# Performance work log

Measured on AMD Instinct MI355X. Metric: run time of the kernel, lower is better.

## Reference

```python
import jax, jax.numpy as jnp
import numpy as np

# --- hash-grid / Field hyperparams (from init_kwargs defaults) ---
L = 16            # n_levels
F = 2             # n_features_per_level
LOG2_T = 19
T = 1 << LOG2_T   # hashmap size per level
NMIN = 16         # base_resolution
MAXRES = 512
SCALE = 1.0
HIDDEN = 32
OUT_DIM = 1
N = 2_000_000
B = float(np.exp(np.log(MAXRES * SCALE / NMIN) / (L - 1)))  # per_level_scale
PRIMES = jnp.array([1, 2654435761, 805459861], dtype=jnp.uint32)
# 8 corner offsets of the unit cube, (8,3)
CORNERS = jnp.array([[(c >> 0) & 1, (c >> 1) & 1, (c >> 2) & 1] for c in range(8)], dtype=jnp.uint32)


def hash_encode(xn, table):
    """xn: (N,3) in [0,1]; table: (L,T,F). Returns (N, L*F)."""
    feats = []
    for l in range(L):  # fixed small loop over levels
        s = NMIN * (B ** l) - 1.0          # tcnn-style grid scale
        pos = xn * s                        # (N,3)
        p0 = jnp.floor(pos)
        w = pos - p0                        # trilinear fracs, (N,3)
        p0i = p0.astype(jnp.uint32)
        corner = p0i[:, None, :] + CORNERS[None, :, :]          # (N,8,3)
        h = corner * PRIMES                                      # (N,8,3) uint32 wrap-mul
        idx = (h[..., 0] ^ h[..., 1] ^ h[..., 2]) & jnp.uint32(T - 1)  # (N,8)
        # trilinear weights per corner: prod over dims of w or (1-w)
        cw = jnp.where(CORNERS[None, :, :] == 1, w[:, None, :], 1.0 - w[:, None, :])
        cw = cw.prod(axis=-1)                                    # (N,8)
        g = table[l][idx.astype(jnp.int32)]                      # (N,8,F)
        feats.append(jnp.einsum('ncf,nc->nf', g, cw))            # (N,F)
    return jnp.concatenate(feats, axis=-1)                       # (N, L*F)


def setup_inputs() -> dict:
    key = jax.random.key(0)
    ks = jax.random.split(key, 8)
    x = jax.random.uniform(ks[0], (N, 3), jnp.float32)  # coords in [0,1) subset of [-scale,scale]
    table = jax.random.normal(ks[1], (L, T, F), jnp.float32) * 1e-2
    W0 = jax.random.normal(ks[2], (L * F + 3, HIDDEN), jnp.float32) * 0.1
    b0 = jnp.zeros((HIDDEN,), jnp.float32)
    W1 = jax.random.normal(ks[3], (HIDDEN, HIDDEN), jnp.float32) * 0.1
    b1 = jnp.zeros((HIDDEN,), jnp.float32)
    Wout = jax.random.normal(ks[4], (HIDDEN, OUT_DIM), jnp.float32) * 0.1
    bout = jnp.zeros((OUT_DIM,), jnp.float32)
    return {"x": x, "table": table, "W0": W0, "b0": b0, "W1": W1, "b1": b1, "Wout": Wout, "bout": bout}


def reference(x, table, W0, b0, W1, b1, Wout, bout):
    # density(): normalize coords to [0,1]
    xn = (x + SCALE) / (2.0 * SCALE)
    # back_prop=0: encoder sees detached coords
    h = hash_encode(jax.lax.stop_gradient(xn), table)   # (N, L*F)
    feat = jnp.concatenate([xn, h], axis=-1)            # (N, 35)  torch.cat([x, h], 1)
    h1 = jax.nn.elu(feat @ W0 + b0)
    h2 = jax.nn.elu(h1 @ W1 + b1)
    out = h2 @ Wout + bout                              # (N, 1)
    return out
```

## Files before the change

kernel.cpp:

```cpp
#include <hip/hip_runtime.h>
#include <hip/hip_fp16.h>
#include <cmath>

#define LVL   16
#define NDENSE 11
#define NHASH  (LVL - NDENSE)
#define TSIZE (1u << 19)
#define TMASK (TSIZE - 1u)
#define HID   32
#define PRIME1 2654435761u
#define PRIME2 805459861u
#define FSTRIDE 72

struct Scales { float s[LVL]; };
struct DenseInfo {
    int X0[NDENSE];
    int dim[NDENSE];
    int dimsq[NDENSE];
    int base[NDENSE];
    int eoff[NDENSE + 1];
};

typedef _Float16 f16x8 __attribute__((ext_vector_type(8)));
typedef float    f32x4 __attribute__((ext_vector_type(4)));
typedef float    f32x2 __attribute__((ext_vector_type(2)));
typedef unsigned u32x4 __attribute__((ext_vector_type(4)));

__device__ __forceinline__ float elu_f(float v) {
    return v > 0.0f ? v : expm1f(v);
}
__device__ __forceinline__ unsigned sel4(u32x4 v, unsigned s) {
    unsigned lo = (s & 1) ? v.y : v.x;
    unsigned hi = (s & 1) ? v.w : v.z;
    return (s & 2) ? hi : lo;
}
__device__ __forceinline__ unsigned hashed(unsigned cx, unsigned cy, unsigned cz) {
    return (cx ^ (cy * PRIME1) ^ (cz * PRIME2)) & TMASK;
}

__device__ __forceinline__ unsigned enc8(float v) {
    unsigned short t = __half_as_ushort(__float2half_rn(v * 0.0625f));
    unsigned m = (unsigned)(t & 0x7FFF) + 0x40u;
    return ((t >> 8) & 0x80u) | (m >> 7);
}
__device__ __forceinline__ float2 dec2(unsigned hw) {
    unsigned h2 = ((hw & 0x8000u) << 16) | ((hw & 0x7F00u) << 15)
                | ((hw & 0x80u)   << 8)  | ((hw & 0x7Fu)   << 7);
    __half2 hh; __builtin_memcpy(&hh, &h2, 4);
    return __half22float2(hh);
}

__global__ __launch_bounds__(256)
void convert_hash8(const f32x2* __restrict__ src, unsigned short* __restrict__ dst)
{
    int i = blockIdx.x * blockDim.x + threadIdx.x;
    if (i >= NHASH * (int)TSIZE) return;
    int l = NDENSE + i / (int)TSIZE;
    int s = i & (int)TMASK;
    f32x2 v = src[(size_t)l * TSIZE + s];
    dst[i] = (unsigned short)(enc8(v.x) | (enc8(v.y) << 8));
}

__global__ __launch_bounds__(256)
void dense_prep8(const float* __restrict__ table, u32x4* __restrict__ dtab,
                 DenseInfo di)
{
    int e = blockIdx.x * blockDim.x + threadIdx.x;
    if (e >= di.eoff[NDENSE]) return;
    int l = 0;
#pragma unroll
    for (int k = 1; k < NDENSE; ++k) if (e >= di.eoff[k]) l = k;
    int le = e - di.eoff[l];
    int D = di.dim[l];
    int ex = le % D; int r = le / D;
    int ey = r % D;  int ez = r / D;
    unsigned cx = (unsigned)(di.X0[l] + ex);
    unsigned cy = (unsigned)(di.X0[l] + ey);
    unsigned cz = (unsigned)(di.X0[l] + ez);
    const f32x2* __restrict__ tl = (const f32x2*)table + (size_t)l * TSIZE;
    f32x2 c0 = tl[hashed(cx,      cy,      cz)];
    f32x2 c1 = tl[hashed(cx + 1u, cy,      cz)];
    f32x2 c2 = tl[hashed(cx,      cy + 1u, cz)];
    f32x2 c3 = tl[hashed(cx + 1u, cy + 1u, cz)];
    f32x2 c4 = tl[hashed(cx,      cy,      cz + 1u)];
    f32x2 c5 = tl[hashed(cx + 1u, cy,      cz + 1u)];
    f32x2 c6 = tl[hashed(cx,      cy + 1u, cz + 1u)];
    f32x2 c7 = tl[hashed(cx + 1u, cy + 1u, cz + 1u)];
    u32x4 q;
    q.x = enc8(c0.x) | (enc8(c0.y) << 8) | (enc8(c1.x) << 16) | (enc8(c1.y) << 24);
    q.y = enc8(c2.x) | (enc8(c2.y) << 8) | (enc8(c3.x) << 16) | (enc8(c3.y) << 24);
    q.z = enc8(c4.x) | (enc8(c4.y) << 8) | (enc8(c5.x) << 16) | (enc8(c5.y) << 24);
    q.w = enc8(c6.x) | (enc8(c6.y) << 8) | (enc8(c7.x) << 16) | (enc8(c7.y) << 24);
    dtab[di.base[l] + le] = q;
}

__global__ void prep_frags(const float* __restrict__ W0, const float* __restrict__ W1,
                           const float* __restrict__ Wout, _Float16* __restrict__ frags)
{
    int idx = blockIdx.x * blockDim.x + threadIdx.x;
    if (idx >= 14*64*8) return;
    int f = idx >> 9;
    int rem = idx & 511;
    int lane = rem >> 3;
    int j = rem & 7;
    int q = lane >> 4;
    int nn = lane & 15;

    float w = 0.0f;
    bool lo;
    if (f < 8) {
        int part = f >> 2, kt = (f >> 1) & 1, nt = f & 1;
        int k = kt*32 + q*8 + j;
        int ncol = nt*16 + nn;
        float val = 0.0f;
        if (k < 32)      val = W0[(3 + k)  * HID + ncol];
        else if (k < 35) val = W0[(k - 32) * HID + ncol];
        else if (k < 38) val = W0[(k - 35) * HID + ncol];
        w = val; lo = (part == 1);
    } else if (f < 12) {
        int part = (f - 8) >> 1, nt = (f - 8) & 1;
        int k = q*8 + j;
        int ncol = nt*16 + nn;
        w = W1[k * HID + ncol]; lo = (part == 1);
    } else {
        int part = f - 12;
        int k = q*8 + j;
        w = (nn == 0) ? Wout[k] : 0.0f; lo = (part == 1);
    }
    _Float16 hi = (_Float16)w;
    frags[idx] = lo ? (_Float16)(w - (float)hi) : hi;
}

__global__ __launch_bounds__(256, 4)
void fused_mfma_kernel(const float* __restrict__ x, const u32x4* __restrict__ htab8,
                       const u32x4* __restrict__ dtab,
                       const float* __restrict__ b0, const float* __restrict__ b1,
                       const float* __restrict__ bout, const _Float16* __restrict__ fragbuf,
                       float* __restrict__ out, int n, Scales sc, DenseInfo di)
{
    __shared__ __attribute__((aligned(16))) _Float16 featL[256 * FSTRIDE];
    __shared__ __attribute__((aligned(16))) _Float16 h1h[4][16*32], h1l[4][16*32];
    __shared__ __attribute__((aligned(16))) _Float16 h2h[4][16*32], h2l[4][16*32];

    const int t = threadIdx.x;
    const int pbase = blockIdx.x * 256;
    const int p  = pbase + t;
    const int pc = p < n ? p : n - 1;

    const float xn0 = (x[3*pc+0] + 1.0f) * 0.5f;
    const float xn1 = (x[3*pc+1] + 1.0f) * 0.5f;
    const float xn2 = (x[3*pc+2] + 1.0f) * 0.5f;

    _Float16* row = &featL[t * FSTRIDE];
    {
        _Float16 h0 = (_Float16)xn0, h1_ = (_Float16)xn1, h2_ = (_Float16)xn2;
        row[32] = h0; row[33] = h1_; row[34] = h2_;
        row[35] = (_Float16)(xn0 - (float)h0);
        row[36] = (_Float16)(xn1 - (float)h1_);
        row[37] = (_Float16)(xn2 - (float)h2_);
#pragma unroll
        for (int k = 38; k < 64; ++k) row[k] = (_Float16)0.0f;
    }

#pragma unroll
    for (int l = 0; l < NDENSE; ++l) {
        const float s = sc.s[l];
        float px = xn0 * s, py = xn1 * s, pz = xn2 * s;
        float fx = floorf(px), fy = floorf(py), fz = floorf(pz);
        float wx = px - fx, wy = py - fy, wz = pz - fz;
        int D = di.dim[l], Dsq = di.dimsq[l], X0 = di.X0[l];
        int cx = (int)fx - X0, cy = (int)fy - X0, cz = (int)fz - X0;
        cx = min(max(cx, 0), D - 1);
        cy = min(max(cy, 0), D - 1);
        cz = min(max(cz, 0), D - 1);
        u32x4 Q = dtab[(size_t)(di.base[l] + cx + cy * D + cz * Dsq)];
        float2 a00 = dec2(Q.x & 0xFFFFu), a10 = dec2(Q.x >> 16);
        float2 a01 = dec2(Q.y & 0xFFFFu), a11 = dec2(Q.y >> 16);
        float2 c00 = dec2(Q.z & 0xFFFFu), c10 = dec2(Q.z >> 16);
        float2 c01 = dec2(Q.w & 0xFFFFu), c11 = dec2(Q.w >> 16);
        float ux = 1.0f - wx, uy = 1.0f - wy, uz = 1.0f - wz;
        float b0x = uy*(ux*a00.x + wx*a10.x) + wy*(ux*a01.x + wx*a11.x);
        float b0y = uy*(ux*a00.y + wx*a10.y) + wy*(ux*a01.y + wx*a11.y);
        float b1x = uy*(ux*c00.x + wx*c10.x) + wy*(ux*c01.x + wx*c11.x);
        float b1y = uy*(ux*c00.y + wx*c10.y) + wy*(ux*c01.y + wx*c11.y);
        row[2*l + 0] = (_Float16)(16.0f * (uz * b0x + wz * b1x));
        row[2*l + 1] = (_Float16)(16.0f * (uz * b0y + wz * b1y));
    }

#pragma unroll
    for (int l = NDENSE; l < LVL; ++l) {
        const u32x4* __restrict__ qt = htab8 + ((size_t)(l - NDENSE) * TSIZE >> 3);
        const float s = sc.s[l];
        float px = xn0 * s, py = xn1 * s, pz = xn2 * s;
        float fx = floorf(px), fy = floorf(py), fz = floorf(pz);
        float wx = px - fx, wy = py - fy, wz = pz - fz;
        unsigned x0 = (unsigned)fx, y0 = (unsigned)fy, z0 = (unsigned)fz;
        unsigned hy0 = y0 * PRIME1, hy1 = hy0 + PRIME1;
        unsigned hz0 = z0 * PRIME2, hz1 = hz0 + PRIME2;
        unsigned b00 = hy0 ^ hz0, b10 = hy1 ^ hz0, b01 = hy0 ^ hz1, b11 = hy1 ^ hz1;
        unsigned i0 = (x0 ^ b00) & TMASK;
        unsigned i1 = (x0 ^ b10) & TMASK;
        unsigned i2 = (x0 ^ b01) & TMASK;
        unsigned i3 = (x0 ^ b11) & TMASK;

        u32x4 Q0 = qt[i0 >> 3];
        u32x4 Q1 = qt[i1 >> 3];
        u32x4 Q2 = qt[i2 >> 3];
        u32x4 Q3 = qt[i3 >> 3];

        unsigned dm = (x0 ^ (x0 + 1u)) & TMASK;
        unsigned j0 = i0 ^ dm, j1 = i1 ^ dm, j2 = i2 ^ dm, j3 = i3 ^ dm;

        unsigned hc0, hc1, hc2, hc3;
        if ((x0 & 7u) == 7u) {
            u32x4 R0 = qt[j0 >> 3];
            u32x4 R1 = qt[j1 >> 3];
            u32x4 R2 = qt[j2 >> 3];
            u32x4 R3 = qt[j3 >> 3];
            unsigned d0 = sel4(R0, (j0 >> 1) & 3), d1 = sel4(R1, (j1 >> 1) & 3);
            unsigned d2 = sel4(R2, (j2 >> 1) & 3), d3 = sel4(R3, (j3 >> 1) & 3);
            hc0 = (j0 & 1) ? (d0 >> 16) : (d0 & 0xFFFFu);
            hc1 = (j1 & 1) ? (d1 >> 16) : (d1 & 0xFFFFu);
            hc2 = (j2 & 1) ? (d2 >> 16) : (d2 & 0xFFFFu);
            hc3 = (j3 & 1) ? (d3 >> 16) : (d3 & 0xFFFFu);
        } else {
            unsigned d0 = sel4(Q0, (j0 >> 1) & 3), d1 = sel4(Q1, (j1 >> 1) & 3);
            unsigned d2 = sel4(Q2, (j2 >> 1) & 3), d3 = sel4(Q3, (j3 >> 1) & 3);
            hc0 = (j0 & 1) ? (d0 >> 16) : (d0 & 0xFFFFu);
            hc1 = (j1 & 1) ? (d1 >> 16) : (d1 & 0xFFFFu);
            hc2 = (j2 & 1) ? (d2 >> 16) : (d2 & 0xFFFFu);
            hc3 = (j3 & 1) ? (d3 >> 16) : (d3 & 0xFFFFu);
        }
        unsigned e0 = sel4(Q0, (i0 >> 1) & 3), e1 = sel4(Q1, (i1 >> 1) & 3);
        unsigned e2 = sel4(Q2, (i2 >> 1) & 3), e3 = sel4(Q3, (i3 >> 1) & 3);
        unsigned ha0 = (i0 & 1) ? (e0 >> 16) : (e0 & 0xFFFFu);
        unsigned ha1 = (i1 & 1) ? (e1 >> 16) : (e1 & 0xFFFFu);
        unsigned ha2 = (i2 & 1) ? (e2 >> 16) : (e2 & 0xFFFFu);
        unsigned ha3 = (i3 & 1) ? (e3 >> 16) : (e3 & 0xFFFFu);

        float2 A0 = dec2(ha0), A1 = dec2(ha1), A2 = dec2(ha2), A3 = dec2(ha3);
        float2 C0 = dec2(hc0), C1 = dec2(hc1), C2 = dec2(hc2), C3 = dec2(hc3);
        float ux = 1.0f - wx, uy = 1.0f - wy, uz = 1.0f - wz;
        float w00 = uy*uz, w10 = wy*uz, w01 = uy*wz, w11 = wy*wz;
        float f0 = ux * (w00*A0.x + w10*A1.x + w01*A2.x + w11*A3.x)
                 + wx * (w00*C0.x + w10*C1.x + w01*C2.x + w11*C3.x);
        float f1 = ux * (w00*A0.y + w10*A1.y + w01*A2.y + w11*A3.y)
                 + wx * (w00*C0.y + w10*C1.y + w01*C2.y + w11*C3.y);

        row[2*l + 0] = (_Float16)(16.0f * f0);
        row[2*l + 1] = (_Float16)(16.0f * f1);
    }
    __syncthreads();

    const int l = t & 63, w = t >> 6;
    const int q = l >> 4, nn = l & 15;

    const f16x8* FB = (const f16x8*)fragbuf;
    f16x8 B0h00 = FB[0*64 + l], B0h01 = FB[1*64 + l];
    f16x8 B0h10 = FB[2*64 + l], B0h11 = FB[3*64 + l];
    f16x8 B0l00 = FB[4*64 + l], B0l01 = FB[5*64 + l];
    f16x8 B0l10 = FB[6*64 + l], B0l11 = FB[7*64 + l];
    f16x8 B1h0  = FB[8*64 + l], B1h1  = FB[9*64 + l];
    f16x8 B1l0  = FB[10*64 + l], B1l1 = FB[11*64 + l];
    f16x8 B2h   = FB[12*64 + l], B2l  = FB[13*64 + l];

    float bias00 = b0[nn], bias01 = b0[16 + nn];
    float bias10 = b1[nn], bias11 = b1[16 + nn];
    float biasO  = (nn == 0) ? bout[0] : 0.0f;

    _Float16* H1h = &h1h[w][0]; _Float16* H1l = &h1l[w][0];
    _Float16* H2h = &h2h[w][0]; _Float16* H2l = &h2l[w][0];

#pragma unroll
    for (int mt = 0; mt < 4; ++mt) {
        const int mrow = w*64 + mt*16 + nn;
        const _Float16* arow = &featL[mrow * FSTRIDE];

        f16x8 A0 = *(const f16x8*)(arow + q*8);
        f16x8 A1 = *(const f16x8*)(arow + 32 + q*8);
        f32x4 c0 = {bias00, bias00, bias00, bias00};
        f32x4 c1 = {bias01, bias01, bias01, bias01};
        c0 = __builtin_amdgcn_mfma_f32_16x16x32_f16(A0, B0h00, c0, 0, 0, 0);
        c0 = __builtin_amdgcn_mfma_f32_16x16x32_f16(A1, B0h10, c0, 0, 0, 0);
        c0 = __builtin_amdgcn_mfma_f32_16x16x32_f16(A0, B0l00, c0, 0, 0, 0);
        c0 = __builtin_amdgcn_mfma_f32_16x16x32_f16(A1, B0l10, c0, 0, 0, 0);
        c1 = __builtin_amdgcn_mfma_f32_16x16x32_f16(A0, B0h01, c1, 0, 0, 0);
        c1 = __builtin_amdgcn_mfma_f32_16x16x32_f16(A1, B0h11, c1, 0, 0, 0);
        c1 = __builtin_amdgcn_mfma_f32_16x16x32_f16(A0, B0l01, c1, 0, 0, 0);
        c1 = __builtin_amdgcn_mfma_f32_16x16x32_f16(A1, B0l11, c1, 0, 0, 0);

#pragma unroll
        for (int r = 0; r < 4; ++r) {
            int m = q*4 + r;
            float e0 = elu_f(c0[r]);
            _Float16 hh = (_Float16)e0;
            H1h[m*32 + nn]      = hh;
            H1l[m*32 + nn]      = (_Float16)(e0 - (float)hh);
            float e1 = elu_f(c1[r]);
            hh = (_Float16)e1;
            H1h[m*32 + 16 + nn] = hh;
            H1l[m*32 + 16 + nn] = (_Float16)(e1 - (float)hh);
        }

        f16x8 Ah = *(const f16x8*)(H1h + nn*32 + q*8);
        f16x8 Al = *(const f16x8*)(H1l + nn*32 + q*8);
        f32x4 d0 = {bias10, bias10, bias10, bias10};
        f32x4 d1 = {bias11, bias11, bias11, bias11};
        d0 = __builtin_amdgcn_mfma_f32_16x16x32_f16(Ah, B1h0, d0, 0, 0, 0);
        d0 = __builtin_amdgcn_mfma_f32_16x16x32_f16(Ah, B1l0, d0, 0, 0, 0);
        d0 = __builtin_amdgcn_mfma_f32_16x16x32_f16(Al, B1h0, d0, 0, 0, 0);
        d1 = __builtin_amdgcn_mfma_f32_16x16x32_f16(Ah, B1h1, d1, 0, 0, 0);
        d1 = __builtin_amdgcn_mfma_f32_16x16x32_f16(Ah, B1l1, d1, 0, 0, 0);
        d1 = __builtin_amdgcn_mfma_f32_16x16x32_f16(Al, B1h1, d1, 0, 0, 0);

#pragma unroll
        for (int r = 0; r < 4; ++r) {
            int m = q*4 + r;
            float e0 = elu_f(d0[r]);
            _Float16 hh = (_Float16)e0;
            H2h[m*32 + nn]      = hh;
            H2l[m*32 + nn]      = (_Float16)(e0 - (float)hh);
            float e1 = elu_f(d1[r]);
            hh = (_Float16)e1;
            H2h[m*32 + 16 + nn] = hh;
            H2l[m*32 + 16 + nn] = (_Float16)(e1 - (float)hh);
        }

        f16x8 A2h = *(const f16x8*)(H2h + nn*32 + q*8);
        f16x8 A2l = *(const f16x8*)(H2l + nn*32 + q*8);
        f32x4 c3 = {biasO, biasO, biasO, biasO};
        c3 = __builtin_amdgcn_mfma_f32_16x16x32_f16(A2h, B2h, c3, 0, 0, 0);
        c3 = __builtin_amdgcn_mfma_f32_16x16x32_f16(A2h, B2l, c3, 0, 0, 0);
        c3 = __builtin_amdgcn_mfma_f32_16x16x32_f16(A2l, B2h, c3, 0, 0, 0);

        if (nn == 0) {
            int pout = pbase + w*64 + mt*16 + q*4;
#pragma unroll
            for (int r = 0; r < 4; ++r)
                if (pout + r < n) out[pout + r] = c3[r];
        }
    }
}

__device__ __forceinline__ float2 enc_level_f32(float xn0, float xn1, float xn2, float s,
                                                const float2* __restrict__ tb)
{
    float px = xn0 * s, py = xn1 * s, pz = xn2 * s;
    float fx = floorf(px), fy = floorf(py), fz = floorf(pz);
    float wx = px - fx, wy = py - fy, wz = pz - fz;
    unsigned x0 = (unsigned)fx, y0 = (unsigned)fy, z0 = (unsigned)fz;
    unsigned hy0 = y0 * PRIME1, hy1 = hy0 + PRIME1;
    unsigned hz0 = z0 * PRIME2, hz1 = hz0 + PRIME2;
    unsigned b00 = hy0 ^ hz0, b10 = hy1 ^ hz0, b01 = hy0 ^ hz1, b11 = hy1 ^ hz1;
    float2 g000 = tb[( x0       ^ b00) & TMASK];
    float2 g100 = tb[((x0 + 1u) ^ b00) & TMASK];
    float2 g010 = tb[( x0       ^ b10) & TMASK];
    float2 g110 = tb[((x0 + 1u) ^ b10) & TMASK];
    float2 g001 = tb[( x0       ^ b01) & TMASK];
    float2 g101 = tb[((x0 + 1u) ^ b01) & TMASK];
    float2 g011 = tb[( x0       ^ b11) & TMASK];
    float2 g111 = tb[((x0 + 1u) ^ b11) & TMASK];
    float ux = 1.0f - wx, uy = 1.0f - wy, uz = 1.0f - wz;
    float c00 = uy*uz, c10 = wy*uz, c01 = uy*wz, c11 = wy*wz;
    float f0 = ux * (c00*g000.x + c10*g010.x + c01*g001.x + c11*g011.x)
             + wx * (c00*g100.x + c10*g110.x + c01*g101.x + c11*g111.x);
    float f1 = ux * (c00*g000.y + c10*g010.y + c01*g001.y + c11*g011.y)
             + wx * (c00*g100.y + c10*g110.y + c01*g101.y + c11*g111.y);
    return make_float2(f0, f1);
}

__global__ __launch_bounds__(256, 4)
void fused_fp32_kernel(const float* __restrict__ x, const float* __restrict__ table,
                       const float* __restrict__ W0, const float* __restrict__ b0,
                       const float* __restrict__ W1, const float* __restrict__ b1,
                       const float* __restrict__ Wout, const float* __restrict__ bout,
                       float* __restrict__ out, int n, Scales sc)
{
    int tid = blockIdx.x * blockDim.x + threadIdx.x;
    if (tid >= n) return;
    float xn0 = (x[3*tid+0] + 1.0f) * 0.5f;
    float xn1 = (x[3*tid+1] + 1.0f) * 0.5f;
    float xn2 = (x[3*tid+2] + 1.0f) * 0.5f;
    float acc[HID];
#pragma unroll
    for (int j = 0; j < HID; ++j)
        acc[j] = b0[j] + xn0 * W0[0*HID + j] + xn1 * W0[1*HID + j] + xn2 * W0[2*HID + j];
#pragma unroll
    for (int lv = 0; lv < LVL; ++lv) {
        const float2* tb = (const float2*)table + (size_t)lv * TSIZE;
        float2 f = enc_level_f32(xn0, xn1, xn2, sc.s[lv], tb);
        const float* w0r0 = W0 + (3 + 2*lv) * HID;
        const float* w0r1 = W0 + (4 + 2*lv) * HID;
#pragma unroll
        for (int j = 0; j < HID; ++j)
            acc[j] += f.x * w0r0[j] + f.y * w0r1[j];
    }
#pragma unroll
    for (int j = 0; j < HID; ++j) acc[j] = elu_f(acc[j]);
    float acc2[HID];
#pragma unroll
    for (int j = 0; j < HID; ++j) acc2[j] = b1[j];
#pragma unroll
    for (int k = 0; k < HID; ++k) {
        float hk = acc[k];
        const float* w1r = W1 + k * HID;
#pragma unroll
        for (int j = 0; j < HID; ++j) acc2[j] += hk * w1r[j];
    }
    float o = bout[0];
#pragma unroll
    for (int k = 0; k < HID; ++k) o += elu_f(acc2[k]) * Wout[k];
    out[tid] = o;
}

extern "C" void kernel_launch(void* const* d_in, const int* in_sizes, int n_in,
                              void* d_out, int out_size, void* d_ws, size_t ws_size,
                              hipStream_t stream)
{
    const float* x    = (const float*)d_in[0];
    const float* tb   = (const float*)d_in[1];
    const float* W0   = (const float*)d_in[2];
    const float* b0   = (const float*)d_in[3];
    const float* W1   = (const float*)d_in[4];
    const float* b1   = (const float*)d_in[5];
    const float* Wout = (const float*)d_in[6];
    const float* bo   = (const float*)d_in[7];
    float* out = (float*)d_out;

    int n = in_sizes[0] / 3;

    Scales sc;
    DenseInfo di;
    double B = exp(log(32.0) / 15.0);
    {
        int base = 0, ecum = 0;
        for (int l = 0; l < LVL; ++l) {
            double sd = 16.0 * pow(B, (double)l) - 1.0;
            sc.s[l] = (float)sd;
            if (l < NDENSE) {
                int X0   = (int)floor(0.5 * sd) - 2; if (X0 < 0) X0 = 0;
                int Xmax = (int)ceil(sd) + 2;
                int dim  = Xmax - X0 + 1;
                di.X0[l] = X0; di.dim[l] = dim; di.dimsq[l] = dim * dim;
                di.base[l] = base; di.eoff[l] = ecum;
                base += dim * dim * dim;
                ecum += dim * dim * dim;
            }
        }
        di.eoff[NDENSE] = ecum;
    }

    const size_t dense_bytes = (size_t)di.eoff[NDENSE] * 16;
    const size_t hash8_bytes = (size_t)NHASH * TSIZE * 2;
    const size_t frag_bytes  = 14 * 64 * 8 * sizeof(_Float16);
    int block = 256;
    int pgrid = (n + block - 1) / block;

    if (ws_size >= dense_bytes + hash8_bytes + frag_bytes) {
        u32x4*          dtab  = (u32x4*)d_ws;
        unsigned short* htab8 = (unsigned short*)((char*)d_ws + dense_bytes);
        _Float16*       frags = (_Float16*)((char*)d_ws + dense_bytes + hash8_bytes);
        int hgrid = (NHASH * (int)TSIZE + block - 1) / block;
        convert_hash8<<<hgrid, block, 0, stream>>>((const f32x2*)tb, htab8);
        int dgrid = (di.eoff[NDENSE] + block - 1) / block;
        dense_prep8<<<dgrid, block, 0, stream>>>(tb, dtab, di);
        prep_frags<<<28, 256, 0, stream>>>(W0, W1, Wout, frags);
        fused_mfma_kernel<<<pgrid, block, 0, stream>>>(x, (const u32x4*)htab8, dtab,
                                                       b0, b1, bo, frags, out, n, sc, di);
    } else {
        fused_fp32_kernel<<<pgrid, block, 0, stream>>>(x, tb, W0, b0, W1, b1, Wout, bo, out, n, sc);
    }
}
```

Measured before the change: 522.7 us.

## Switch tables to hardware FP8, software-pipeline hash loads, split dense table build

Table entries are now encoded with the hardware FP8 pack/unpack conversion instructions instead of the hand-rolled 8-bit half truncation. The dense-level build is split into a per-grid-point kernel followed by a cell-gather kernel, which uses the output buffer as scratch. In the main kernel, all dense-level loads are issued up front and the hash-level loads are software-pipelined three levels deep with 32-bit gathers. The feature tile uses an XOR-swizzled 64-wide layout written as 16-byte vectors, the second hidden layer reuses the first layer's LDS buffers, and ELU uses fast __expf. Together these aim to cut memory latency, preprocessing gathers, LDS bank conflicts and ALU work, at the cost of more registers and changed precision.

```diff
diff --git a/kernel.cpp b/kernel.cpp
--- a/kernel.cpp
+++ b/kernel.cpp
@@ -10,7 +10,6 @@
 #define HID   32
 #define PRIME1 2654435761u
 #define PRIME2 805459861u
-#define FSTRIDE 72
 
 struct Scales { float s[LVL]; };
 struct DenseInfo {
@@ -20,6 +19,11 @@
     int base[NDENSE];
     int eoff[NDENSE + 1];
 };
+struct PtInfo {
+    int P1[NDENSE];
+    int pbase[NDENSE];
+    int ptotal;
+};
 
 typedef _Float16 f16x8 __attribute__((ext_vector_type(8)));
 typedef float    f32x4 __attribute__((ext_vector_type(4)));
@@ -27,27 +31,28 @@
 typedef unsigned u32x4 __attribute__((ext_vector_type(4)));
 
 __device__ __forceinline__ float elu_f(float v) {
-    return v > 0.0f ? v : expm1f(v);
-}
-__device__ __forceinline__ unsigned sel4(u32x4 v, unsigned s) {
-    unsigned lo = (s & 1) ? v.y : v.x;
-    unsigned hi = (s & 1) ? v.w : v.z;
-    return (s & 2) ? hi : lo;
+    return v > 0.0f ? v : __expf(v) - 1.0f;
 }
 __device__ __forceinline__ unsigned hashed(unsigned cx, unsigned cy, unsigned cz) {
     return (cx ^ (cy * PRIME1) ^ (cz * PRIME2)) & TMASK;
 }
 
-__device__ __forceinline__ unsigned enc8(float v) {
-    unsigned short t = __half_as_ushort(__float2half_rn(v * 0.0625f));
-    unsigned m = (unsigned)(t & 0x7FFF) + 0x40u;
-    return ((t >> 8) & 0x80u) | (m >> 7);
-}
-__device__ __forceinline__ float2 dec2(unsigned hw) {
-    unsigned h2 = ((hw & 0x8000u) << 16) | ((hw & 0x7F00u) << 15)
-                | ((hw & 0x80u)   << 8)  | ((hw & 0x7Fu)   << 7);
-    __half2 hh; __builtin_memcpy(&hh, &h2, 4);
-    return __half22float2(hh);
+__device__ __forceinline__ unsigned enc_pair(float a, float b) {
+    return ((unsigned)__builtin_amdgcn_cvt_pk_fp8_f32(a * 64.0f, b * 64.0f, 0, false)) & 0xFFFFu;
+}
+__device__ __forceinline__ f32x2 dec_lo(unsigned d) {
+    return __builtin_amdgcn_cvt_pk_f32_fp8((int)d, false);
+}
+__device__ __forceinline__ f32x2 dec_hi(unsigned d) {
+    return __builtin_amdgcn_cvt_pk_f32_fp8((int)d, true);
+}
+__device__ __forceinline__ unsigned pack_ff(_Float16 a, _Float16 b) {
+    unsigned short ua = __builtin_bit_cast(unsigned short, a);
+    unsigned short ub = __builtin_bit_cast(unsigned short, b);
+    return (unsigned)ua | ((unsigned)ub << 16);
+}
+__device__ __forceinline__ unsigned pack_f2(f32x2 f) {
+    return pack_ff((_Float16)f.x, (_Float16)f.y);
 }
 
 __global__ __launch_bounds__(256)
@@ -58,7 +63,58 @@
     int l = NDENSE + i / (int)TSIZE;
     int s = i & (int)TMASK;
     f32x2 v = src[(size_t)l * TSIZE + s];
-    dst[i] = (unsigned short)(enc8(v.x) | (enc8(v.y) << 8));
+    dst[i] = (unsigned short)enc_pair(v.x, v.y);
+}
+
+__global__ __launch_bounds__(256)
+void dense_pts(const float* __restrict__ table, unsigned short* __restrict__ pts,
+               DenseInfo di, PtInfo pi)
+{
+    int p = blockIdx.x * blockDim.x + threadIdx.x;
+    if (p >= pi.ptotal) return;
+    int l = 0;
+#pragma unroll
+    for (int k = 1; k < NDENSE; ++k) if (p >= pi.pbase[k]) l = k;
+    int X0 = 0, D1 = 1, pb = 0;
+#pragma unroll
+    for (int k = 0; k < NDENSE; ++k)
+        if (l == k) { X0 = di.X0[k]; D1 = pi.P1[k]; pb = pi.pbase[k]; }
+    int lp = p - pb;
+    int x = lp % D1; int r = lp / D1;
+    int y = r % D1;  int z = r / D1;
+    unsigned cx = (unsigned)(X0 + x), cy = (unsigned)(X0 + y), cz = (unsigned)(X0 + z);
+    const f32x2* __restrict__ tl = (const f32x2*)table + (size_t)l * TSIZE;
+    f32x2 v = tl[hashed(cx, cy, cz)];
+    pts[p] = (unsigned short)enc_pair(v.x, v.y);
+}
+
+__global__ __launch_bounds__(256)
+void dense_cells(const unsigned short* __restrict__ pts, u32x4* __restrict__ dtab,
+                 DenseInfo di, PtInfo pi)
+{
+    int e = blockIdx.x * blockDim.x + threadIdx.x;
+    if (e >= di.eoff[NDENSE]) return;
+    int l = 0;
+#pragma unroll
+    for (int k = 1; k < NDENSE; ++k) if (e >= di.eoff[k]) l = k;
+    int D = 1, D1 = 1, base = 0, eo = 0, pb = 0;
+#pragma unroll
+    for (int k = 0; k < NDENSE; ++k)
+        if (l == k) { D = di.dim[k]; D1 = pi.P1[k]; base = di.base[k]; eo = di.eoff[k]; pb = pi.pbase[k]; }
+    int le = e - eo;
+    int ex = le % D; int r = le / D;
+    int ey = r % D;  int ez = r / D;
+    const unsigned short* __restrict__ q = pts + pb;
+    int i00 = ex + (ey + ez * D1) * D1;
+    int i01 = i00 + D1;
+    int i10 = i00 + D1 * D1;
+    int i11 = i10 + D1;
+    u32x4 Q;
+    Q.x = (unsigned)q[i00] | ((unsigned)q[i00 + 1] << 16);
+    Q.y = (unsigned)q[i01] | ((unsigned)q[i01 + 1] << 16);
+    Q.z = (unsigned)q[i10] | ((unsigned)q[i10 + 1] << 16);
+    Q.w = (unsigned)q[i11] | ((unsigned)q[i11 + 1] << 16);
+    dtab[base + le] = Q;
 }
 
 __global__ __launch_bounds__(256)
@@ -70,13 +126,16 @@
     int l = 0;
 #pragma unroll
     for (int k = 1; k < NDENSE; ++k) if (e >= di.eoff[k]) l = k;
-    int le = e - di.eoff[l];
-    int D = di.dim[l];
+    int X0 = 0, D = 1, base = 0, eo = 0;
+#pragma unroll
+    for (int k = 0; k < NDENSE; ++k)
+        if (l == k) { X0 = di.X0[k]; D = di.dim[k]; base = di.base[k]; eo = di.eoff[k]; }
+    int le = e - eo;
     int ex = le % D; int r = le / D;
     int ey = r % D;  int ez = r / D;
-    unsigned cx = (unsigned)(di.X0[l] + ex);
-    unsigned cy = (unsigned)(di.X0[l] + ey);
-    unsigned cz = (unsigned)(di.X0[l] + ez);
+    unsigned cx = (unsigned)(X0 + ex);
+    unsigned cy = (unsigned)(X0 + ey);
+    unsigned cz = (unsigned)(X0 + ez);
     const f32x2* __restrict__ tl = (const f32x2*)table + (size_t)l * TSIZE;
     f32x2 c0 = tl[hashed(cx,      cy,      cz)];
     f32x2 c1 = tl[hashed(cx + 1u, cy,      cz)];
@@ -86,12 +145,12 @@
     f32x2 c5 = tl[hashed(cx + 1u, cy,      cz + 1u)];
     f32x2 c6 = tl[hashed(cx,      cy + 1u, cz + 1u)];
     f32x2 c7 = tl[hashed(cx + 1u, cy + 1u, cz + 1u)];
-    u32x4 q;
-    q.x = enc8(c0.x) | (enc8(c0.y) << 8) | (enc8(c1.x) << 16) | (enc8(c1.y) << 24);
-    q.y = enc8(c2.x) | (enc8(c2.y) << 8) | (enc8(c3.x) << 16) | (enc8(c3.y) << 24);
-    q.z = enc8(c4.x) | (enc8(c4.y) << 8) | (enc8(c5.x) << 16) | (enc8(c5.y) << 24);
-    q.w = enc8(c6.x) | (enc8(c6.y) << 8) | (enc8(c7.x) << 16) | (enc8(c7.y) << 24);
-    dtab[di.base[l] + le] = q;
+    u32x4 Q;
+    Q.x = enc_pair(c0.x, c0.y) | (enc_pair(c1.x, c1.y) << 16);
+    Q.y = enc_pair(c2.x, c2.y) | (enc_pair(c3.x, c3.y) << 16);
+    Q.z = enc_pair(c4.x, c4.y) | (enc_pair(c5.x, c5.y) << 16);
+    Q.w = enc_pair(c6.x, c6.y) | (enc_pair(c7.x, c7.y) << 16);
+    dtab[base + le] = Q;
 }
 
 __global__ void prep_frags(const float* __restrict__ W0, const float* __restrict__ W1,
@@ -131,16 +190,64 @@
     frags[idx] = lo ? (_Float16)(w - (float)hi) : hi;
 }
 
+struct HL {
+    unsigned d0, d1, d2, d3;
+    unsigned e0, e1, e2, e3;
+    unsigned i0, i1, i2, i3, dm;
+    float wx, wy, wz;
+};
+
+__device__ __forceinline__ void hash_issue(HL& h, const unsigned* __restrict__ hq,
+                                           float xn0, float xn1, float xn2, float s)
+{
+    float px = xn0 * s, py = xn1 * s, pz = xn2 * s;
+    float fx = floorf(px), fy = floorf(py), fz = floorf(pz);
+    h.wx = px - fx; h.wy = py - fy; h.wz = pz - fz;
+    unsigned x0 = (unsigned)fx, y0 = (unsigned)fy, z0 = (unsigned)fz;
+    unsigned hy0 = y0 * PRIME1, hy1 = hy0 + PRIME1;
+    unsigned hz0 = z0 * PRIME2, hz1 = hz0 + PRIME2;
+    unsigned b00 = hy0 ^ hz0, b10 = hy1 ^ hz0, b01 = hy0 ^ hz1, b11 = hy1 ^ hz1;
+    h.i0 = (x0 ^ b00) & TMASK;
+    h.i1 = (x0 ^ b10) & TMASK;
+    h.i2 = (x0 ^ b01) & TMASK;
+    h.i3 = (x0 ^ b11) & TMASK;
+    h.dm = (x0 ^ (x0 + 1u)) & TMASK;
+    h.d0 = hq[h.i0 >> 1]; h.d1 = hq[h.i1 >> 1];
+    h.d2 = hq[h.i2 >> 1]; h.d3 = hq[h.i3 >> 1];
+    unsigned j0 = h.i0 ^ h.dm, j1 = h.i1 ^ h.dm, j2 = h.i2 ^ h.dm, j3 = h.i3 ^ h.dm;
+    h.e0 = hq[j0 >> 1]; h.e1 = hq[j1 >> 1];
+    h.e2 = hq[j2 >> 1]; h.e3 = hq[j3 >> 1];
+}
+
+__device__ __forceinline__ unsigned pick_hw(unsigned d, unsigned idx) {
+    return (idx & 1u) ? (d >> 16) : (d & 0xFFFFu);
+}
+
+__device__ __forceinline__ f32x2 hash_consume(const HL& h)
+{
+    f32x2 A0 = dec_lo(pick_hw(h.d0, h.i0)), A1 = dec_lo(pick_hw(h.d1, h.i1));
+    f32x2 A2 = dec_lo(pick_hw(h.d2, h.i2)), A3 = dec_lo(pick_hw(h.d3, h.i3));
+    unsigned j0 = h.i0 ^ h.dm, j1 = h.i1 ^ h.dm, j2 = h.i2 ^ h.dm, j3 = h.i3 ^ h.dm;
+    f32x2 C0 = dec_lo(pick_hw(h.e0, j0)), C1 = dec_lo(pick_hw(h.e1, j1));
+    f32x2 C2 = dec_lo(pick_hw(h.e2, j2)), C3 = dec_lo(pick_hw(h.e3, j3));
+    float uy  = 1.0f - h.wy;
+    float uzs = (1.0f - h.wz) * 0.015625f;
+    float wzs = h.wz * 0.015625f;
+    float w00 = uy * uzs, w10 = h.wy * uzs, w01 = uy * wzs, w11 = h.wy * wzs;
+    f32x2 a = A0 * w00 + A1 * w10 + A2 * w01 + A3 * w11;
+    f32x2 c = C0 * w00 + C1 * w10 + C2 * w01 + C3 * w11;
+    return a * (1.0f - h.wx) + c * h.wx;
+}
+
 __global__ __launch_bounds__(256, 4)
-void fused_mfma_kernel(const float* __restrict__ x, const u32x4* __restrict__ htab8,
+void fused_mfma_kernel(const float* __restrict__ x, const unsigned* __restrict__ htab,
                        const u32x4* __restrict__ dtab,
                        const float* __restrict__ b0, const float* __restrict__ b1,
                        const float* __restrict__ bout, const _Float16* __restrict__ fragbuf,
                        float* __restrict__ out, int n, Scales sc, DenseInfo di)
 {
-    __shared__ __attribute__((aligned(16))) _Float16 featL[256 * FSTRIDE];
+    __shared__ __attribute__((aligned(16))) _Float16 featL[256 * 64];
     __shared__ __attribute__((aligned(16))) _Float16 h1h[4][16*32], h1l[4][16*32];
-    __shared__ __attribute__((aligned(16))) _Float16 h2h[4][16*32], h2l[4][16*32];
 
     const int t = threadIdx.x;
     const int pbase = blockIdx.x * 256;
@@ -151,133 +258,101 @@
     const float xn1 = (x[3*pc+1] + 1.0f) * 0.5f;
     const float xn2 = (x[3*pc+2] + 1.0f) * 0.5f;
 
-    _Float16* row = &featL[t * FSTRIDE];
-    {
-        _Float16 h0 = (_Float16)xn0, h1_ = (_Float16)xn1, h2_ = (_Float16)xn2;
-        row[32] = h0; row[33] = h1_; row[34] = h2_;
-        row[35] = (_Float16)(xn0 - (float)h0);
-        row[36] = (_Float16)(xn1 - (float)h1_);
-        row[37] = (_Float16)(xn2 - (float)h2_);
-#pragma unroll
-        for (int k = 38; k < 64; ++k) row[k] = (_Float16)0.0f;
-    }
+    u32x4 qd[NDENSE];
+#pragma unroll
+    for (int l = 0; l < NDENSE; ++l) {
+        const float s = sc.s[l];
+        int D = di.dim[l];
+        int cx = (int)floorf(xn0 * s) - di.X0[l];
+        int cy = (int)floorf(xn1 * s) - di.X0[l];
+        int cz = (int)floorf(xn2 * s) - di.X0[l];
+        cx = min(max(cx, 0), D - 1);
+        cy = min(max(cy, 0), D - 1);
+        cz = min(max(cz, 0), D - 1);
+        qd[l] = dtab[(size_t)(di.base[l] + cx + cy * D + cz * di.dimsq[l])];
+    }
+
+    HL hA, hB, hC;
+    hash_issue(hA, htab + 0 * (TSIZE / 2), xn0, xn1, xn2, sc.s[11]);
+    hash_issue(hB, htab + 1 * (TSIZE / 2), xn0, xn1, xn2, sc.s[12]);
+    hash_issue(hC, htab + 2 * (TSIZE / 2), xn0, xn1, xn2, sc.s[13]);
+
+    unsigned rr[LVL];
 
 #pragma unroll
     for (int l = 0; l < NDENSE; ++l) {
         const float s = sc.s[l];
         float px = xn0 * s, py = xn1 * s, pz = xn2 * s;
-        float fx = floorf(px), fy = floorf(py), fz = floorf(pz);
-        float wx = px - fx, wy = py - fy, wz = pz - fz;
-        int D = di.dim[l], Dsq = di.dimsq[l], X0 = di.X0[l];
-        int cx = (int)fx - X0, cy = (int)fy - X0, cz = (int)fz - X0;
-        cx = min(max(cx, 0), D - 1);
-        cy = min(max(cy, 0), D - 1);
-        cz = min(max(cz, 0), D - 1);
-        u32x4 Q = dtab[(size_t)(di.base[l] + cx + cy * D + cz * Dsq)];
-        float2 a00 = dec2(Q.x & 0xFFFFu), a10 = dec2(Q.x >> 16);
-        float2 a01 = dec2(Q.y & 0xFFFFu), a11 = dec2(Q.y >> 16);
-        float2 c00 = dec2(Q.z & 0xFFFFu), c10 = dec2(Q.z >> 16);
-        float2 c01 = dec2(Q.w & 0xFFFFu), c11 = dec2(Q.w >> 16);
-        float ux = 1.0f - wx, uy = 1.0f - wy, uz = 1.0f - wz;
-        float b0x = uy*(ux*a00.x + wx*a10.x) + wy*(ux*a01.x + wx*a11.x);
-        float b0y = uy*(ux*a00.y + wx*a10.y) + wy*(ux*a01.y + wx*a11.y);
-        float b1x = uy*(ux*c00.x + wx*c10.x) + wy*(ux*c01.x + wx*c11.x);
-        float b1y = uy*(ux*c00.y + wx*c10.y) + wy*(ux*c01.y + wx*c11.y);
-        row[2*l + 0] = (_Float16)(16.0f * (uz * b0x + wz * b1x));
-        row[2*l + 1] = (_Float16)(16.0f * (uz * b0y + wz * b1y));
-    }
-
-#pragma unroll
-    for (int l = NDENSE; l < LVL; ++l) {
-        const u32x4* __restrict__ qt = htab8 + ((size_t)(l - NDENSE) * TSIZE >> 3);
-        const float s = sc.s[l];
-        float px = xn0 * s, py = xn1 * s, pz = xn2 * s;
-        float fx = floorf(px), fy = floorf(py), fz = floorf(pz);
-        float wx = px - fx, wy = py - fy, wz = pz - fz;
-        unsigned x0 = (unsigned)fx, y0 = (unsigned)fy, z0 = (unsigned)fz;
-        unsigned hy0 = y0 * PRIME1, hy1 = hy0 + PRIME1;
-        unsigned hz0 = z0 * PRIME2, hz1 = hz0 + PRIME2;
-        unsigned b00 = hy0 ^ hz0, b10 = hy1 ^ hz0, b01 = hy0 ^ hz1, b11 = hy1 ^ hz1;
-        unsigned i0 = (x0 ^ b00) & TMASK;
-        unsigned i1 = (x0 ^ b10) & TMASK;
-        unsigned i2 = (x0 ^ b01) & TMASK;
-        unsigned i3 = (x0 ^ b11) & TMASK;
-
-        u32x4 Q0 = qt[i0 >> 3];
-        u32x4 Q1 = qt[i1 >> 3];
-        u32x4 Q2 = qt[i2 >> 3];
-        u32x4 Q3 = qt[i3 >> 3];
-
-        unsigned dm = (x0 ^ (x0 + 1u)) & TMASK;
-        unsigned j0 = i0 ^ dm, j1 = i1 ^ dm, j2 = i2 ^ dm, j3 = i3 ^ dm;
-
-        unsigned hc0, hc1, hc2, hc3;
-        if ((x0 & 7u) == 7u) {
-            u32x4 R0 = qt[j0 >> 3];
-            u32x4 R1 = qt[j1 >> 3];
-            u32x4 R2 = qt[j2 >> 3];
-            u32x4 R3 = qt[j3 >> 3];
-            unsigned d0 = sel4(R0, (j0 >> 1) & 3), d1 = sel4(R1, (j1 >> 1) & 3);
-            unsigned d2 = sel4(R2, (j2 >> 1) & 3), d3 = sel4(R3, (j3 >> 1) & 3);
-            hc0 = (j0 & 1) ? (d0 >> 16) : (d0 & 0xFFFFu);
-            hc1 = (j1 & 1) ? (d1 >> 16) : (d1 & 0xFFFFu);
-            hc2 = (j2 & 1) ? (d2 >> 16) : (d2 & 0xFFFFu);
-            hc3 = (j3 & 1) ? (d3 >> 16) : (d3 & 0xFFFFu);
-        } else {
-            unsigned d0 = sel4(Q0, (j0 >> 1) & 3), d1 = sel4(Q1, (j1 >> 1) & 3);
-            unsigned d2 = sel4(Q2, (j2 >> 1) & 3), d3 = sel4(Q3, (j3 >> 1) & 3);
-            hc0 = (j0 & 1) ? (d0 >> 16) : (d0 & 0xFFFFu);
-            hc1 = (j1 & 1) ? (d1 >> 16) : (d1 & 0xFFFFu);
-            hc2 = (j2 & 1) ? (d2 >> 16) : (d2 & 0xFFFFu);
-            hc3 = (j3 & 1) ? (d3 >> 16) : (d3 & 0xFFFFu);
-        }
-        unsigned e0 = sel4(Q0, (i0 >> 1) & 3), e1 = sel4(Q1, (i1 >> 1) & 3);
-        unsigned e2 = sel4(Q2, (i2 >> 1) & 3), e3 = sel4(Q3, (i3 >> 1) & 3);
-        unsigned ha0 = (i0 & 1) ? (e0 >> 16) : (e0 & 0xFFFFu);
-        unsigned ha1 = (i1 & 1) ? (e1 >> 16) : (e1 & 0xFFFFu);
-        unsigned ha2 = (i2 & 1) ? (e2 >> 16) : (e2 & 0xFFFFu);
-        unsigned ha3 = (i3 & 1) ? (e3 >> 16) : (e3 & 0xFFFFu);
-
-        float2 A0 = dec2(ha0), A1 = dec2(ha1), A2 = dec2(ha2), A3 = dec2(ha3);
-        float2 C0 = dec2(hc0), C1 = dec2(hc1), C2 = dec2(hc2), C3 = dec2(hc3);
-        float ux = 1.0f - wx, uy = 1.0f - wy, uz = 1.0f - wz;
-        float w00 = uy*uz, w10 = wy*uz, w01 = uy*wz, w11 = wy*wz;
-        float f0 = ux * (w00*A0.x + w10*A1.x + w01*A2.x + w11*A3.x)
-                 + wx * (w00*C0.x + w10*C1.x + w01*C2.x + w11*C3.x);
-        float f1 = ux * (w00*A0.y + w10*A1.y + w01*A2.y + w11*A3.y)
-                 + wx * (w00*C0.y + w10*C1.y + w01*C2.y + w11*C3.y);
-
-        row[2*l + 0] = (_Float16)(16.0f * f0);
-        row[2*l + 1] = (_Float16)(16.0f * f1);
-    }
-    __syncthreads();
-
-    const int l = t & 63, w = t >> 6;
-    const int q = l >> 4, nn = l & 15;
+        float wx = px - floorf(px), wy = py - floorf(py), wz = pz - floorf(pz);
+        u32x4 Q = qd[l];
+        f32x2 a00 = dec_lo(Q.x), a10 = dec_hi(Q.x);
+        f32x2 a01 = dec_lo(Q.y), a11 = dec_hi(Q.y);
+        f32x2 c00 = dec_lo(Q.z), c10 = dec_hi(Q.z);
+        f32x2 c01 = dec_lo(Q.w), c11 = dec_hi(Q.w);
+        float ux = 1.0f - wx, uy = 1.0f - wy;
+        float uzs = (1.0f - wz) * 0.015625f, wzs = wz * 0.015625f;
+        f32x2 t0 = a00 * ux + a10 * wx;
+        f32x2 t1 = a01 * ux + a11 * wx;
+        f32x2 t2 = c00 * ux + c10 * wx;
+        f32x2 t3 = c01 * ux + c11 * wx;
+        f32x2 u0 = t0 * uy + t1 * wy;
+        f32x2 u1 = t2 * uy + t3 * wy;
+        f32x2 f  = u0 * uzs + u1 * wzs;
+        rr[l] = pack_f2(f);
+    }
+
+    rr[11] = pack_f2(hash_consume(hA));
+    hash_issue(hA, htab + 3 * (TSIZE / 2), xn0, xn1, xn2, sc.s[14]);
+    rr[12] = pack_f2(hash_consume(hB));
+    hash_issue(hB, htab + 4 * (TSIZE / 2), xn0, xn1, xn2, sc.s[15]);
+    rr[13] = pack_f2(hash_consume(hC));
+    rr[14] = pack_f2(hash_consume(hA));
+    rr[15] = pack_f2(hash_consume(hB));
+
+    {
+        u32x4* fl = (u32x4*)&featL[t * 64];
+        const int swt = t & 7;
+        u32x4 ch;
+        ch.x = rr[0];  ch.y = rr[1];  ch.z = rr[2];  ch.w = rr[3];  fl[0 ^ swt] = ch;
+        ch.x = rr[4];  ch.y = rr[5];  ch.z = rr[6];  ch.w = rr[7];  fl[1 ^ swt] = ch;
+        ch.x = rr[8];  ch.y = rr[9];  ch.z = rr[10]; ch.w = rr[11]; fl[2 ^ swt] = ch;
+        ch.x = rr[12]; ch.y = rr[13]; ch.z = rr[14]; ch.w = rr[15]; fl[3 ^ swt] = ch;
+        _Float16 X0h = (_Float16)xn0, X1h = (_Float16)xn1, X2h = (_Float16)xn2;
+        _Float16 L0h = (_Float16)(xn0 - (float)X0h);
+        _Float16 L1h = (_Float16)(xn1 - (float)X1h);
+        _Float16 L2h = (_Float16)(xn2 - (float)X2h);
+        ch.x = pack_ff(X0h, X1h); ch.y = pack_ff(X2h, L0h);
+        ch.z = pack_ff(L1h, L2h); ch.w = 0;
+        fl[4 ^ swt] = ch;
+        u32x4 Z; Z.x = 0; Z.y = 0; Z.z = 0; Z.w = 0;
+        fl[5 ^ swt] = Z; fl[6 ^ swt] = Z; fl[7 ^ swt] = Z;
+    }
+
+    const int lane = t & 63, w = t >> 6;
+    const int q = lane >> 4, nn = lane & 15;
 
     const f16x8* FB = (const f16x8*)fragbuf;
-    f16x8 B0h00 = FB[0*64 + l], B0h01 = FB[1*64 + l];
-    f16x8 B0h10 = FB[2*64 + l], B0h11 = FB[3*64 + l];
-    f16x8 B0l00 = FB[4*64 + l], B0l01 = FB[5*64 + l];
-    f16x8 B0l10 = FB[6*64 + l], B0l11 = FB[7*64 + l];
-    f16x8 B1h0  = FB[8*64 + l], B1h1  = FB[9*64 + l];
-    f16x8 B1l0  = FB[10*64 + l], B1l1 = FB[11*64 + l];
-    f16x8 B2h   = FB[12*64 + l], B2l  = FB[13*64 + l];
+    f16x8 B0h00 = FB[0*64 + lane], B0h01 = FB[1*64 + lane];
+    f16x8 B0h10 = FB[2*64 + lane], B0h11 = FB[3*64 + lane];
+    f16x8 B0l00 = FB[4*64 + lane], B0l01 = FB[5*64 + lane];
+    f16x8 B0l10 = FB[6*64 + lane], B0l11 = FB[7*64 + lane];
+    f16x8 B1h0  = FB[8*64 + lane], B1h1  = FB[9*64 + lane];
+    f16x8 B1l0  = FB[10*64 + lane], B1l1 = FB[11*64 + lane];
+    f16x8 B2h   = FB[12*64 + lane], B2l  = FB[13*64 + lane];
 
     float bias00 = b0[nn], bias01 = b0[16 + nn];
     float bias10 = b1[nn], bias11 = b1[16 + nn];
     float biasO  = (nn == 0) ? bout[0] : 0.0f;
 
     _Float16* H1h = &h1h[w][0]; _Float16* H1l = &h1l[w][0];
-    _Float16* H2h = &h2h[w][0]; _Float16* H2l = &h2l[w][0];
 
 #pragma unroll
     for (int mt = 0; mt < 4; ++mt) {
         const int mrow = w*64 + mt*16 + nn;
-        const _Float16* arow = &featL[mrow * FSTRIDE];
-
-        f16x8 A0 = *(const f16x8*)(arow + q*8);
-        f16x8 A1 = *(const f16x8*)(arow + 32 + q*8);
+        const f16x8* ar = (const f16x8*)&featL[mrow * 64];
+        f16x8 A0 = ar[q ^ (nn & 7)];
+        f16x8 A1 = ar[(4 + q) ^ (nn & 7)];
+
         f32x4 c0 = {bias00, bias00, bias00, bias00};
         f32x4 c1 = {bias01, bias01, bias01, bias01};
         c0 = __builtin_amdgcn_mfma_f32_16x16x32_f16(A0, B0h00, c0, 0, 0, 0);
@@ -318,16 +393,16 @@
             int m = q*4 + r;
             float e0 = elu_f(d0[r]);
             _Float16 hh = (_Float16)e0;
-            H2h[m*32 + nn]      = hh;
-            H2l[m*32 + nn]      = (_Float16)(e0 - (float)hh);
+            H1h[m*32 + nn]      = hh;
+            H1l[m*32 + nn]      = (_Float16)(e0 - (float)hh);
             float e1 = elu_f(d1[r]);
             hh = (_Float16)e1;
-            H2h[m*32 + 16 + nn] = hh;
-            H2l[m*32 + 16 + nn] = (_Float16)(e1 - (float)hh);
+            H1h[m*32 + 16 + nn] = hh;
+            H1l[m*32 + 16 + nn] = (_Float16)(e1 - (float)hh);
         }
 
-        f16x8 A2h = *(const f16x8*)(H2h + nn*32 + q*8);
-        f16x8 A2l = *(const f16x8*)(H2l + nn*32 + q*8);
+        f16x8 A2h = *(const f16x8*)(H1h + nn*32 + q*8);
+        f16x8 A2l = *(const f16x8*)(H1l + nn*32 + q*8);
         f32x4 c3 = {biasO, biasO, biasO, biasO};
         c3 = __builtin_amdgcn_mfma_f32_16x16x32_f16(A2h, B2h, c3, 0, 0, 0);
         c3 = __builtin_amdgcn_mfma_f32_16x16x32_f16(A2h, B2l, c3, 0, 0, 0);
@@ -431,9 +506,10 @@
 
     Scales sc;
     DenseInfo di;
+    PtInfo pi;
     double B = exp(log(32.0) / 15.0);
     {
-        int base = 0, ecum = 0;
+        int base = 0, ecum = 0, pcum = 0;
         for (int l = 0; l < LVL; ++l) {
             double sd = 16.0 * pow(B, (double)l) - 1.0;
             sc.s[l] = (float)sd;
@@ -445,9 +521,13 @@
                 di.base[l] = base; di.eoff[l] = ecum;
                 base += dim * dim * dim;
                 ecum += dim * dim * dim;
+                int D1 = dim + 1;
+                pi.P1[l] = D1; pi.pbase[l] = pcum;
+                pcum += D1 * D1 * D1;
             }
         }
         di.eoff[NDENSE] = ecum;
+        pi.ptotal = pcum;
     }
 
     const size_t dense_bytes = (size_t)di.eoff[NDENSE] * 16;
@@ -460,12 +540,23 @@
         u32x4*          dtab  = (u32x4*)d_ws;
         unsigned short* htab8 = (unsigned short*)((char*)d_ws + dense_bytes);
         _Float16*       frags = (_Float16*)((char*)d_ws + dense_bytes + hash8_bytes);
+
         int hgrid = (NHASH * (int)TSIZE + block - 1) / block;
         convert_hash8<<<hgrid, block, 0, stream>>>((const f32x2*)tb, htab8);
-        int dgrid = (di.eoff[NDENSE] + block - 1) / block;
-        dense_prep8<<<dgrid, block, 0, stream>>>(tb, dtab, di);
+
+        if ((size_t)out_size >= (size_t)pi.ptotal * 2) {
+            unsigned short* pts = (unsigned short*)d_out;
+            int ptg = (pi.ptotal + block - 1) / block;
+            dense_pts<<<ptg, block, 0, stream>>>(tb, pts, di, pi);
+            int clg = (di.eoff[NDENSE] + block - 1) / block;
+            dense_cells<<<clg, block, 0, stream>>>(pts, dtab, di, pi);
+        } else {
+            int dgrid = (di.eoff[NDENSE] + block - 1) / block;
+            dense_prep8<<<dgrid, block, 0, stream>>>(tb, dtab, di);
+        }
+
         prep_frags<<<28, 256, 0, stream>>>(W0, W1, Wout, frags);
-        fused_mfma_kernel<<<pgrid, block, 0, stream>>>(x, (const u32x4*)htab8, dtab,
+        fused_mfma_kernel<<<pgrid, block, 0, stream>>>(x, (const unsigned*)htab8, dtab,
                                                        b0, b1, bo, frags, out, n, sc, di);
     } else {
         fused_fp32_kernel<<<pgrid, block, 0, stream>>>(x, tb, W0, b0, W1, b1, Wout, bo, out, n, sc);
```

Result: slower. 626.2 us (+19.8%).
